# Performance work log

Measured on AMD Instinct MI355X. Metric: run time of the kernel, lower is better.

Reference implementation:

```python
import jax, jax.numpy as jnp
import numpy as np

N_NODES = 50000
N_EDGES = 600000
NODE_DIM = 128
HIDDEN = 128
LN_EPS = 1e-5


def setup_inputs() -> dict:
    key = jax.random.key(0)
    ks = jax.random.split(key, 12)
    x = jax.random.normal(ks[0], (N_NODES, NODE_DIM), dtype=jnp.float32)
    edge_index = jax.random.randint(ks[1], (2, N_EDGES), 0, N_NODES, dtype=jnp.int32)
    # GCNConv weights (glorot-ish scaling)
    W1 = jax.random.normal(ks[2], (NODE_DIM, HIDDEN), dtype=jnp.float32) / np.sqrt(NODE_DIM)
    b1 = jnp.zeros((HIDDEN,), jnp.float32)
    W2 = jax.random.normal(ks[3], (HIDDEN, HIDDEN), dtype=jnp.float32) / np.sqrt(HIDDEN)
    b2 = jnp.zeros((HIDDEN,), jnp.float32)
    g1 = jnp.ones((HIDDEN,), jnp.float32)
    beta1 = jnp.zeros((HIDDEN,), jnp.float32)
    g2 = jnp.ones((HIDDEN,), jnp.float32)
    beta2 = jnp.zeros((HIDDEN,), jnp.float32)
    return {"x": x, "edge_index": edge_index, "W1": W1, "b1": b1, "g1": g1,
            "beta1": beta1, "W2": W2, "b2": b2, "g2": g2, "beta2": beta2}


def _gcn_conv(x, src, dst, norm, W, b, n):
    # x' = sum_{j->i} norm_ji * (x_j @ W) + b   (self-loops already in src/dst)
    h = x @ W                                   # [N, H]
    msg = h[src] * norm[:, None]                # [E+N, H]
    out = jax.ops.segment_sum(msg, dst, num_segments=n)
    return out + b


def _layer_norm(x, gamma, beta):
    mu = jnp.mean(x, axis=-1, keepdims=True)
    var = jnp.mean((x - mu) ** 2, axis=-1, keepdims=True)
    return (x - mu) * jax.lax.rsqrt(var + LN_EPS) * gamma + beta


def reference(x, edge_index, W1, b1, g1, beta1, W2, b2, g2, beta2):
    n = x.shape[0]
    loop = jnp.arange(n, dtype=edge_index.dtype)
    src = jnp.concatenate([edge_index[0], loop])
    dst = jnp.concatenate([edge_index[1], loop])
    # symmetric normalization with self-loops (PyG GCNConv default)
    deg = jax.ops.segment_sum(jnp.ones_like(dst, dtype=x.dtype), dst, num_segments=n)
    dinv = jnp.where(deg > 0, jax.lax.rsqrt(jnp.maximum(deg, 1.0)), 0.0)
    norm = dinv[src] * dinv[dst]                # [E+N]

    h = _gcn_conv(x, src, dst, norm, W1, b1, n)
    h = _layer_norm(h, g1, beta1)
    h = jax.nn.relu(h)                          # relu between layers only
    h = _gcn_conv(h, src, dst, norm, W2, b2, n)
    h = _layer_norm(h, g2, beta2)
    return h
```

## Files before the change

kernel.cpp:

```cpp
#include <hip/hip_runtime.h>

#define DIM 128
#define LN_EPS 1e-5f

typedef __attribute__((ext_vector_type(8))) short bf16x8;
typedef __attribute__((ext_vector_type(4))) float f32x4;

static __device__ __forceinline__ unsigned short f2bf(float f) {
    unsigned int u = __builtin_bit_cast(unsigned int, f);
    u += 0x7fffu + ((u >> 16) & 1u);
    return (unsigned short)(u >> 16);
}
static __device__ __forceinline__ float bf2f_lo(unsigned int u) {
    return __builtin_bit_cast(float, u << 16);
}
static __device__ __forceinline__ float bf2f_hi(unsigned int u) {
    return __builtin_bit_cast(float, u & 0xffff0000u);
}

__global__ __launch_bounds__(256) void wt_count_kernel(const float* __restrict__ W1,
                                                       const float* __restrict__ W2,
                                                       unsigned short* __restrict__ Wt1,
                                                       unsigned short* __restrict__ Wt2,
                                                       const int* __restrict__ dst,
                                                       int* __restrict__ counts, int E) {
    int b = blockIdx.x;
    if (b < 128) {
        int elem = b * 256 + threadIdx.x;
        int which = elem >> 14;
        int rest = elem & 16383;
        int c = rest >> 7;
        int k = rest & 127;
        const float* W = which ? W2 : W1;
        unsigned short* Wt = which ? Wt2 : Wt1;
        Wt[c * 128 + k] = f2bf(W[k * 128 + c]);
    } else {
        int e = (b - 128) * 256 + threadIdx.x;
        if (e < E) atomicAdd(&counts[dst[e]], 1);
    }
}

__global__ __launch_bounds__(256) void scan1_kernel(const int* __restrict__ counts,
                                                    int* __restrict__ tmp,
                                                    int* __restrict__ bsums,
                                                    float* __restrict__ dinv, int n) {
    __shared__ int ts[256];
    int tid = threadIdx.x;
    int base = blockIdx.x * 1024 + tid * 4;
    int v[4];
#pragma unroll
    for (int j = 0; j < 4; ++j) {
        int i = base + j;
        v[j] = (i < n) ? counts[i] : 0;
        if (i < n) dinv[i] = rsqrtf((float)(v[j] + 1));
    }
    int s = v[0] + v[1] + v[2] + v[3];
    ts[tid] = s;
    __syncthreads();
    for (int off = 1; off < 256; off <<= 1) {
        int t2 = (tid >= off) ? ts[tid - off] : 0;
        __syncthreads();
        ts[tid] += t2;
        __syncthreads();
    }
    int excl = ts[tid] - s;
    int pre = excl;
#pragma unroll
    for (int j = 0; j < 4; ++j) {
        int i = base + j;
        if (i < n) tmp[i] = pre;
        pre += v[j];
    }
    if (tid == 255) bsums[blockIdx.x] = ts[255];
}

__global__ __launch_bounds__(256) void scan3_kernel(const int* __restrict__ tmp,
                                                    const int* __restrict__ bsums,
                                                    int* __restrict__ rowptr,
                                                    int* __restrict__ cursor,
                                                    int n, int E, int nb) {
    __shared__ int s_add;
    if (threadIdx.x < 64) {
        int lane = threadIdx.x;
        int v = (lane < nb) ? bsums[lane] : 0;
        int x = v;
#pragma unroll
        for (int off = 1; off < 64; off <<= 1) {
            int y = __shfl_up(x, off);
            if (lane >= off) x += y;
        }
        int excl = x - v;
        int mine = __builtin_amdgcn_readlane(excl, blockIdx.x);
        if (lane == 0) s_add = mine;
    }
    __syncthreads();
    int add = s_add;
    int base = blockIdx.x * 1024 + threadIdx.x * 4;
#pragma unroll
    for (int j = 0; j < 4; ++j) {
        int i = base + j;
        if (i < n) {
            int val = tmp[i] + add;
            rowptr[i] = val;
            cursor[i] = val;
        }
    }
    if (blockIdx.x == 0 && threadIdx.x == 0) rowptr[n] = E;
}

__global__ __launch_bounds__(256) void gemm1_fill_kernel(const float* __restrict__ A,
                                                         const unsigned short* __restrict__ Bt,
                                                         const float* __restrict__ dinv,
                                                         unsigned short* __restrict__ H,
                                                         int n, int ntiles, int gG,
                                                         const int* __restrict__ src,
                                                         const int* __restrict__ dst,
                                                         int* __restrict__ cursor,
                                                         unsigned short* __restrict__ colsrc,
                                                         int E) {
    __shared__ unsigned short Wlds[128 * 136];
    if (blockIdx.x >= gG) {
        int e = (blockIdx.x - gG) * 256 + threadIdx.x;
        if (e < E) {
            int p = atomicAdd(&cursor[dst[e]], 1);
            colsrc[p] = (unsigned short)src[e];
        }
        return;
    }
    for (int u = threadIdx.x; u < 2048; u += 256) {
        int row = u >> 4;
        int sub = u & 15;
        *(bf16x8*)&Wlds[row * 136 + sub * 8] = *(const bf16x8*)(Bt + row * 128 + sub * 8);
    }
    __syncthreads();

    int wid = threadIdx.x >> 6;
    int lane = threadIdx.x & 63;
    int tile = blockIdx.x * 4 + wid;
    if (tile >= ntiles) tile = ntiles - 1;
    int r0 = tile * 16;
    int mrow = lane & 15;
    int kgrp = lane >> 4;

    int arow_i = r0 + mrow;
    if (arow_i > n - 1) arow_i = n - 1;
    const float* arow = A + (size_t)arow_i * DIM + kgrp * 8;

    f32x4 acc[8];
#pragma unroll
    for (int t = 0; t < 8; ++t) acc[t] = (f32x4){0.f, 0.f, 0.f, 0.f};

#pragma unroll
    for (int kc = 0; kc < 4; ++kc) {
        float4 v0 = *(const float4*)(arow + kc * 32);
        float4 v1 = *(const float4*)(arow + kc * 32 + 4);
        bf16x8 af;
        af[0] = (short)f2bf(v0.x); af[1] = (short)f2bf(v0.y);
        af[2] = (short)f2bf(v0.z); af[3] = (short)f2bf(v0.w);
        af[4] = (short)f2bf(v1.x); af[5] = (short)f2bf(v1.y);
        af[6] = (short)f2bf(v1.z); af[7] = (short)f2bf(v1.w);
#pragma unroll
        for (int t = 0; t < 8; ++t) {
            bf16x8 bfv = *(const bf16x8*)&Wlds[(t * 16 + mrow) * 136 + kc * 32 + kgrp * 8];
            acc[t] = __builtin_amdgcn_mfma_f32_16x16x32_bf16(af, bfv, acc[t], 0, 0, 0);
        }
    }

    float dv[4];
#pragma unroll
    for (int reg = 0; reg < 4; ++reg) {
        int rr = r0 + kgrp * 4 + reg;
        dv[reg] = (rr < n) ? dinv[rr] : 0.f;
    }
#pragma unroll
    for (int t = 0; t < 8; ++t) {
#pragma unroll
        for (int reg = 0; reg < 4; ++reg) {
            int row = r0 + kgrp * 4 + reg;
            if (row < n) {
                int col = t * 16 + mrow;
                H[(size_t)row * DIM + col] = f2bf(acc[t][reg] * dv[reg]);
            }
        }
    }
}

__global__ __launch_bounds__(256) void gather_gemm_kernel(const int* __restrict__ rowptr,
                                                          const unsigned short* __restrict__ colsrc,
                                                          const uint4* __restrict__ H4,
                                                          const float* __restrict__ dinv,
                                                          const float* __restrict__ bias,
                                                          const float* __restrict__ gamma,
                                                          const float* __restrict__ beta,
                                                          const unsigned short* __restrict__ Wt2,
                                                          unsigned short* __restrict__ H2,
                                                          int n, int ntiles) {
    __shared__ unsigned short Wlds[128 * 136];
    __shared__ unsigned short Tl[4][16][136];
    for (int u = threadIdx.x; u < 2048; u += 256) {
        int row = u >> 4;
        int sub = u & 15;
        *(bf16x8*)&Wlds[row * 136 + sub * 8] = *(const bf16x8*)(Wt2 + row * 128 + sub * 8);
    }
    __syncthreads();

    int wid = threadIdx.x >> 6;
    int lane = threadIdx.x & 63;
    int tile = blockIdx.x * 4 + wid;
    if (tile >= ntiles) tile = ntiles - 1;
    int r0 = tile * 16;
    int grp = lane >> 4;
    int gl = lane & 15;

    float4 bb0 = ((const float4*)bias)[gl * 2];
    float4 bb1 = ((const float4*)bias)[gl * 2 + 1];
    float4 gg0 = ((const float4*)gamma)[gl * 2];
    float4 gg1 = ((const float4*)gamma)[gl * 2 + 1];
    float4 be0 = ((const float4*)beta)[gl * 2];
    float4 be1 = ((const float4*)beta)[gl * 2 + 1];

    for (int t = 0; t < 4; ++t) {
        int r = r0 + t * 4 + grp;
        int rc = (r < n) ? r : (n - 1);
        float di = dinv[rc];
        uint4 su = H4[(size_t)rc * 16 + gl];
        float a0 = bf2f_lo(su.x), a1 = bf2f_hi(su.x);
        float a2 = bf2f_lo(su.y), a3 = bf2f_hi(su.y);
        float a4 = bf2f_lo(su.z), a5 = bf2f_hi(su.z);
        float a6 = bf2f_lo(su.w), a7 = bf2f_hi(su.w);

        int p0 = rowptr[rc];
        int p1 = rowptr[rc + 1];
        int deg = p1 - p0;
        int m = max(deg, __shfl_xor(deg, 16));
        m = max(m, __shfl_xor(m, 32));
        int nch = (m + 15) >> 4;

        for (int c = 0; c < nch; ++c) {
            int cb = c * 16;
            int gi = p0 + cb + gl;
            gi = gi < p1 ? gi : p1 - 1;
            int idxv = (int)colsrc[gi];

            uint4 h[16];
#pragma unroll
            for (int j = 0; j < 16; ++j) {
                int s = __shfl(idxv, grp * 16 + j);
                h[j] = H4[(size_t)s * 16 + gl];
            }
#pragma unroll
            for (int j = 0; j < 16; ++j) {
                bool act = (cb + j < deg);
                a0 += act ? bf2f_lo(h[j].x) : 0.f;
                a1 += act ? bf2f_hi(h[j].x) : 0.f;
                a2 += act ? bf2f_lo(h[j].y) : 0.f;
                a3 += act ? bf2f_hi(h[j].y) : 0.f;
                a4 += act ? bf2f_lo(h[j].z) : 0.f;
                a5 += act ? bf2f_hi(h[j].z) : 0.f;
                a6 += act ? bf2f_lo(h[j].w) : 0.f;
                a7 += act ? bf2f_hi(h[j].w) : 0.f;
            }
        }

        float v0 = a0 * di + bb0.x;
        float v1 = a1 * di + bb0.y;
        float v2 = a2 * di + bb0.z;
        float v3 = a3 * di + bb0.w;
        float v4 = a4 * di + bb1.x;
        float v5 = a5 * di + bb1.y;
        float v6 = a6 * di + bb1.z;
        float v7 = a7 * di + bb1.w;

        float s1 = v0 + v1 + v2 + v3 + v4 + v5 + v6 + v7;
        float s2 = v0 * v0 + v1 * v1 + v2 * v2 + v3 * v3 +
                   v4 * v4 + v5 * v5 + v6 * v6 + v7 * v7;
#pragma unroll
        for (int off = 8; off > 0; off >>= 1) {
            s1 += __shfl_xor(s1, off);
            s2 += __shfl_xor(s2, off);
        }
        float mu = s1 * (1.f / 128.f);
        float var = s2 * (1.f / 128.f) - mu * mu;
        float rstd = rsqrtf(var + LN_EPS);

        float o0 = fmaxf((v0 - mu) * rstd * gg0.x + be0.x, 0.f);
        float o1 = fmaxf((v1 - mu) * rstd * gg0.y + be0.y, 0.f);
        float o2 = fmaxf((v2 - mu) * rstd * gg0.z + be0.z, 0.f);
        float o3 = fmaxf((v3 - mu) * rstd * gg0.w + be0.w, 0.f);
        float o4 = fmaxf((v4 - mu) * rstd * gg1.x + be1.x, 0.f);
        float o5 = fmaxf((v5 - mu) * rstd * gg1.y + be1.y, 0.f);
        float o6 = fmaxf((v6 - mu) * rstd * gg1.z + be1.z, 0.f);
        float o7 = fmaxf((v7 - mu) * rstd * gg1.w + be1.w, 0.f);

        bf16x8 pk;
        pk[0] = (short)f2bf(o0); pk[1] = (short)f2bf(o1);
        pk[2] = (short)f2bf(o2); pk[3] = (short)f2bf(o3);
        pk[4] = (short)f2bf(o4); pk[5] = (short)f2bf(o5);
        pk[6] = (short)f2bf(o6); pk[7] = (short)f2bf(o7);
        *(bf16x8*)&Tl[wid][t * 4 + grp][gl * 8] = pk;
    }

    __syncthreads();

    int mrow = lane & 15;
    int kg = lane >> 4;
    f32x4 acc[8];
#pragma unroll
    for (int t = 0; t < 8; ++t) acc[t] = (f32x4){0.f, 0.f, 0.f, 0.f};

#pragma unroll
    for (int kc = 0; kc < 4; ++kc) {
        bf16x8 af = *(const bf16x8*)&Tl[wid][mrow][kc * 32 + kg * 8];
#pragma unroll
        for (int t = 0; t < 8; ++t) {
            bf16x8 bfv = *(const bf16x8*)&Wlds[(t * 16 + mrow) * 136 + kc * 32 + kg * 8];
            acc[t] = __builtin_amdgcn_mfma_f32_16x16x32_bf16(af, bfv, acc[t], 0, 0, 0);
        }
    }

    float dv[4];
#pragma unroll
    for (int reg = 0; reg < 4; ++reg) {
        int rr = r0 + kg * 4 + reg;
        dv[reg] = (rr < n) ? dinv[rr] : 0.f;
    }
#pragma unroll
    for (int t = 0; t < 8; ++t) {
#pragma unroll
        for (int reg = 0; reg < 4; ++reg) {
            int row = r0 + kg * 4 + reg;
            if (row < n) {
                int col = t * 16 + mrow;
                H2[(size_t)row * DIM + col] = f2bf(acc[t][reg] * dv[reg]);
            }
        }
    }
}

__global__ __launch_bounds__(256) void gather_ln_kernel(const int* __restrict__ rowptr,
                                                        const unsigned short* __restrict__ colsrc,
                                                        const uint2* __restrict__ H2,
                                                        const float* __restrict__ dinv,
                                                        const float* __restrict__ bias,
                                                        const float* __restrict__ gamma,
                                                        const float* __restrict__ beta,
                                                        uint2* __restrict__ out_bf,
                                                        float* __restrict__ out_f,
                                                        int n, int relu) {
    int wid = threadIdx.x >> 6;
    int lane = threadIdx.x & 63;
    int half = lane >> 5;
    int hl = lane & 31;
    int r = blockIdx.x * 8 + wid * 2 + half;
    int valid = (r < n);
    int rc = valid ? r : (n - 1);

    float di = dinv[rc];
    float4 bb = ((const float4*)bias)[hl];
    float4 gg = ((const float4*)gamma)[hl];
    float4 be = ((const float4*)beta)[hl];

    uint2 su = H2[(size_t)rc * 32 + hl];
    float a0 = bf2f_lo(su.x), a1 = bf2f_hi(su.x);
    float a2 = bf2f_lo(su.y), a3 = bf2f_hi(su.y);

    int p0 = rowptr[rc];
    int p1 = rowptr[rc + 1];
    int deg = p1 - p0;
    int maxd = max(deg, __shfl_xor(deg, 32));
    int nchunks = (maxd + 15) >> 4;
    int hbase = half << 5;

    for (int c = 0; c < nchunks; ++c) {
        int cbase = c * 16;
        int gi = p0 + cbase + hl;
        gi = gi < p1 ? gi : p1 - 1;
        int idxv = (int)colsrc[gi];

        uint2 h[16];
#pragma unroll
        for (int j = 0; j < 16; ++j) {
            int s = __shfl(idxv, hbase + j);
            h[j] = H2[(size_t)s * 32 + hl];
        }
#pragma unroll
        for (int j = 0; j < 16; ++j) {
            bool act = (cbase + j < deg);
            a0 += act ? bf2f_lo(h[j].x) : 0.f;
            a1 += act ? bf2f_hi(h[j].x) : 0.f;
            a2 += act ? bf2f_lo(h[j].y) : 0.f;
            a3 += act ? bf2f_hi(h[j].y) : 0.f;
        }
    }

    float v0 = a0 * di + bb.x;
    float v1 = a1 * di + bb.y;
    float v2 = a2 * di + bb.z;
    float v3 = a3 * di + bb.w;

    float s1 = v0 + v1 + v2 + v3;
    float s2 = v0 * v0 + v1 * v1 + v2 * v2 + v3 * v3;
#pragma unroll
    for (int off = 16; off > 0; off >>= 1) {
        s1 += __shfl_xor(s1, off);
        s2 += __shfl_xor(s2, off);
    }
    float mu = s1 * (1.f / 128.f);
    float var = s2 * (1.f / 128.f) - mu * mu;
    float rstd = rsqrtf(var + LN_EPS);

    float o0 = (v0 - mu) * rstd * gg.x + be.x;
    float o1 = (v1 - mu) * rstd * gg.y + be.y;
    float o2 = (v2 - mu) * rstd * gg.z + be.z;
    float o3 = (v3 - mu) * rstd * gg.w + be.w;
    if (relu) {
        o0 = fmaxf(o0, 0.f); o1 = fmaxf(o1, 0.f);
        o2 = fmaxf(o2, 0.f); o3 = fmaxf(o3, 0.f);
    }
    if (valid) {
        if (out_bf) {
            uint2 pk;
            pk.x = (unsigned int)f2bf(o0) | ((unsigned int)f2bf(o1) << 16);
            pk.y = (unsigned int)f2bf(o2) | ((unsigned int)f2bf(o3) << 16);
            out_bf[(size_t)r * 32 + hl] = pk;
        } else {
            ((float4*)out_f)[(size_t)r * 32 + hl] = make_float4(o0, o1, o2, o3);
        }
    }
}

extern "C" void kernel_launch(void* const* d_in, const int* in_sizes, int n_in,
                              void* d_out, int out_size, void* d_ws, size_t ws_size,
                              hipStream_t stream) {
    const float* x   = (const float*)d_in[0];
    const int*   ei  = (const int*)d_in[1];
    const float* W1  = (const float*)d_in[2];
    const float* b1  = (const float*)d_in[3];
    const float* g1  = (const float*)d_in[4];
    const float* be1 = (const float*)d_in[5];
    const float* W2  = (const float*)d_in[6];
    const float* b2  = (const float*)d_in[7];
    const float* g2  = (const float*)d_in[8];
    const float* be2 = (const float*)d_in[9];

    int n = in_sizes[0] / DIM;
    int E = in_sizes[1] / 2;
    const int* src = ei;
    const int* dst = ei + E;

    char* wp = (char*)d_ws;
    auto alloc = [&](size_t bytes) {
        void* p = (void*)wp;
        wp += (bytes + 255) & ~(size_t)255;
        return p;
    };
    float*          dinv   = (float*)alloc((size_t)n * 4);
    int*            counts = (int*)alloc((size_t)n * 4);
    int*            tmp    = (int*)alloc((size_t)n * 4);
    int*            rowptr = (int*)alloc((size_t)(n + 1) * 4);
    int*            cursor = (int*)alloc((size_t)n * 4);
    int*            bsums  = (int*)alloc(64 * 4);
    unsigned short* colsrc = (unsigned short*)alloc((size_t)E * 2);
    unsigned short* Wt1    = (unsigned short*)alloc(128 * 128 * 2);
    unsigned short* Wt2    = (unsigned short*)alloc(128 * 128 * 2);
    unsigned short* H      = (unsigned short*)alloc((size_t)n * DIM * 2);
    unsigned short* H2     = (unsigned short*)alloc((size_t)n * DIM * 2);

    hipMemsetAsync(counts, 0, (size_t)n * 4, stream);

    int gE = (E + 255) / 256;
    wt_count_kernel<<<128 + gE, 256, 0, stream>>>(W1, W2, Wt1, Wt2, dst, counts, E);

    int nb1 = (n + 1023) / 1024;
    scan1_kernel<<<nb1, 256, 0, stream>>>(counts, tmp, bsums, dinv, n);
    scan3_kernel<<<nb1, 256, 0, stream>>>(tmp, bsums, rowptr, cursor, n, E, nb1);

    int ntiles = (n + 15) / 16;
    int gG = (ntiles + 3) / 4;

    gemm1_fill_kernel<<<gG + gE, 256, 0, stream>>>(x, Wt1, dinv, H, n, ntiles, gG,
                                                   src, dst, cursor, colsrc, E);

    gather_gemm_kernel<<<gG, 256, 0, stream>>>(rowptr, colsrc, (const uint4*)H, dinv,
                                               b1, g1, be1, Wt2, H2, n, ntiles);

    int gA = (n + 7) / 8;
    gather_ln_kernel<<<gA, 256, 0, stream>>>(rowptr, colsrc, (const uint2*)H2, dinv,
                                             b2, g2, be2, nullptr, (float*)d_out, n, 0);
}
```

Measured before the change: 233.4 us.

## Fuse scan kernels with grid sync, shrink gather_gemm blocks, widen final gather

The two prefix-scan kernels become one, where the last block to finish computes the block offsets and the other blocks spin on a flag, so one launch and the tmp round-trip go away. gather_gemm drops the full 34KB W2 copy in LDS and uses 128-thread blocks over 16 rows, with each wave reading half of W2 straight from global memory; this targets higher occupancy at the cost of redundant global reads. The final gather reads 16-byte loads (8 bf16 per lane) with 16 lanes per row instead of 8-byte loads. Bias, gamma and beta loads are moved to where they are used to lower register pressure. The spin-wait relies on all scan blocks being resident at once, which holds for the roughly 49 blocks used here.

```diff
diff --git a/kernel.cpp b/kernel.cpp
--- a/kernel.cpp
+++ b/kernel.cpp
@@ -40,13 +40,18 @@
     }
 }
 
-__global__ __launch_bounds__(256) void scan1_kernel(const int* __restrict__ counts,
-                                                    int* __restrict__ tmp,
-                                                    int* __restrict__ bsums,
-                                                    float* __restrict__ dinv, int n) {
+__global__ __launch_bounds__(256) void scan_fused_kernel(const int* __restrict__ counts,
+                                                         int* __restrict__ bsums,
+                                                         int* __restrict__ bpref,
+                                                         int* __restrict__ sync2,
+                                                         int* __restrict__ rowptr,
+                                                         int* __restrict__ cursor,
+                                                         float* __restrict__ dinv,
+                                                         int n, int E, int nb) {
     __shared__ int ts[256];
     int tid = threadIdx.x;
-    int base = blockIdx.x * 1024 + tid * 4;
+    int b = blockIdx.x;
+    int base = b * 1024 + tid * 4;
     int v[4];
 #pragma unroll
     for (int j = 0; j < 4; ++j) {
@@ -64,48 +69,40 @@
         __syncthreads();
     }
     int excl = ts[tid] - s;
-    int pre = excl;
-#pragma unroll
-    for (int j = 0; j < 4; ++j) {
-        int i = base + j;
-        if (i < n) tmp[i] = pre;
-        pre += v[j];
-    }
-    if (tid == 255) bsums[blockIdx.x] = ts[255];
-}
-
-__global__ __launch_bounds__(256) void scan3_kernel(const int* __restrict__ tmp,
-                                                    const int* __restrict__ bsums,
-                                                    int* __restrict__ rowptr,
-                                                    int* __restrict__ cursor,
-                                                    int n, int E, int nb) {
-    __shared__ int s_add;
-    if (threadIdx.x < 64) {
-        int lane = threadIdx.x;
-        int v = (lane < nb) ? bsums[lane] : 0;
-        int x = v;
-#pragma unroll
-        for (int off = 1; off < 64; off <<= 1) {
-            int y = __shfl_up(x, off);
-            if (lane >= off) x += y;
-        }
-        int excl = x - v;
-        int mine = __builtin_amdgcn_readlane(excl, blockIdx.x);
-        if (lane == 0) s_add = mine;
+
+    if (tid == 255) {
+        bsums[b] = ts[255];
+        __threadfence();
+        int t = atomicAdd(&sync2[0], 1);
+        if (t == nb - 1) {
+            __threadfence();
+            int acc = 0;
+            for (int k = 0; k < nb; ++k) {
+                int sv = bsums[k];
+                bpref[k] = acc;
+                acc += sv;
+            }
+            __threadfence();
+            atomicExch(&sync2[1], 1);
+        }
+    }
+    if (tid == 0) {
+        while (atomicAdd(&sync2[1], 0) == 0) { __builtin_amdgcn_s_sleep(8); }
     }
     __syncthreads();
-    int add = s_add;
-    int base = blockIdx.x * 1024 + threadIdx.x * 4;
+    __threadfence();
+
+    int pre = bpref[b] + excl;
 #pragma unroll
     for (int j = 0; j < 4; ++j) {
         int i = base + j;
         if (i < n) {
-            int val = tmp[i] + add;
-            rowptr[i] = val;
-            cursor[i] = val;
-        }
-    }
-    if (blockIdx.x == 0 && threadIdx.x == 0) rowptr[n] = E;
+            rowptr[i] = pre;
+            cursor[i] = pre;
+        }
+        pre += v[j];
+    }
+    if (b == 0 && tid == 0) rowptr[n] = E;
 }
 
 __global__ __launch_bounds__(256) void gemm1_fill_kernel(const float* __restrict__ A,
@@ -185,52 +182,36 @@
     }
 }
 
-__global__ __launch_bounds__(256) void gather_gemm_kernel(const int* __restrict__ rowptr,
-                                                          const unsigned short* __restrict__ colsrc,
-                                                          const uint4* __restrict__ H4,
-                                                          const float* __restrict__ dinv,
-                                                          const float* __restrict__ bias,
-                                                          const float* __restrict__ gamma,
-                                                          const float* __restrict__ beta,
-                                                          const unsigned short* __restrict__ Wt2,
-                                                          unsigned short* __restrict__ H2,
-                                                          int n, int ntiles) {
-    __shared__ unsigned short Wlds[128 * 136];
-    __shared__ unsigned short Tl[4][16][136];
-    for (int u = threadIdx.x; u < 2048; u += 256) {
-        int row = u >> 4;
-        int sub = u & 15;
-        *(bf16x8*)&Wlds[row * 136 + sub * 8] = *(const bf16x8*)(Wt2 + row * 128 + sub * 8);
-    }
-    __syncthreads();
-
+__global__ __launch_bounds__(128, 5) void gather_gemm_kernel(const int* __restrict__ rowptr,
+                                                             const unsigned short* __restrict__ colsrc,
+                                                             const uint4* __restrict__ H4,
+                                                             const float* __restrict__ dinv,
+                                                             const float* __restrict__ bias,
+                                                             const float* __restrict__ gamma,
+                                                             const float* __restrict__ beta,
+                                                             const unsigned short* __restrict__ Wt2,
+                                                             unsigned short* __restrict__ H2,
+                                                             int n) {
+    __shared__ unsigned short Tl[16][136];
     int wid = threadIdx.x >> 6;
     int lane = threadIdx.x & 63;
-    int tile = blockIdx.x * 4 + wid;
-    if (tile >= ntiles) tile = ntiles - 1;
-    int r0 = tile * 16;
+    int r0 = blockIdx.x * 16;
     int grp = lane >> 4;
     int gl = lane & 15;
 
-    float4 bb0 = ((const float4*)bias)[gl * 2];
-    float4 bb1 = ((const float4*)bias)[gl * 2 + 1];
-    float4 gg0 = ((const float4*)gamma)[gl * 2];
-    float4 gg1 = ((const float4*)gamma)[gl * 2 + 1];
-    float4 be0 = ((const float4*)beta)[gl * 2];
-    float4 be1 = ((const float4*)beta)[gl * 2 + 1];
-
-    for (int t = 0; t < 4; ++t) {
-        int r = r0 + t * 4 + grp;
+#pragma unroll
+    for (int t = 0; t < 2; ++t) {
+        int r = r0 + wid * 8 + t * 4 + grp;
         int rc = (r < n) ? r : (n - 1);
         float di = dinv[rc];
         uint4 su = H4[(size_t)rc * 16 + gl];
+        int p0 = rowptr[rc];
+        int p1 = rowptr[rc + 1];
         float a0 = bf2f_lo(su.x), a1 = bf2f_hi(su.x);
         float a2 = bf2f_lo(su.y), a3 = bf2f_hi(su.y);
         float a4 = bf2f_lo(su.z), a5 = bf2f_hi(su.z);
         float a6 = bf2f_lo(su.w), a7 = bf2f_hi(su.w);
 
-        int p0 = rowptr[rc];
-        int p1 = rowptr[rc + 1];
         int deg = p1 - p0;
         int m = max(deg, __shfl_xor(deg, 16));
         m = max(m, __shfl_xor(m, 32));
@@ -245,8 +226,8 @@
             uint4 h[16];
 #pragma unroll
             for (int j = 0; j < 16; ++j) {
-                int s = __shfl(idxv, grp * 16 + j);
-                h[j] = H4[(size_t)s * 16 + gl];
+                int sS = __shfl(idxv, grp * 16 + j);
+                h[j] = H4[(size_t)sS * 16 + gl];
             }
 #pragma unroll
             for (int j = 0; j < 16; ++j) {
@@ -262,6 +243,8 @@
             }
         }
 
+        float4 bb0 = ((const float4*)bias)[gl * 2];
+        float4 bb1 = ((const float4*)bias)[gl * 2 + 1];
         float v0 = a0 * di + bb0.x;
         float v1 = a1 * di + bb0.y;
         float v2 = a2 * di + bb0.z;
@@ -283,6 +266,11 @@
         float var = s2 * (1.f / 128.f) - mu * mu;
         float rstd = rsqrtf(var + LN_EPS);
 
+        float4 gg0 = ((const float4*)gamma)[gl * 2];
+        float4 gg1 = ((const float4*)gamma)[gl * 2 + 1];
+        float4 be0 = ((const float4*)beta)[gl * 2];
+        float4 be1 = ((const float4*)beta)[gl * 2 + 1];
+
         float o0 = fmaxf((v0 - mu) * rstd * gg0.x + be0.x, 0.f);
         float o1 = fmaxf((v1 - mu) * rstd * gg0.y + be0.y, 0.f);
         float o2 = fmaxf((v2 - mu) * rstd * gg0.z + be0.z, 0.f);
@@ -297,24 +285,25 @@
         pk[2] = (short)f2bf(o2); pk[3] = (short)f2bf(o3);
         pk[4] = (short)f2bf(o4); pk[5] = (short)f2bf(o5);
         pk[6] = (short)f2bf(o6); pk[7] = (short)f2bf(o7);
-        *(bf16x8*)&Tl[wid][t * 4 + grp][gl * 8] = pk;
+        *(bf16x8*)&Tl[wid * 8 + t * 4 + grp][gl * 8] = pk;
     }
 
     __syncthreads();
 
     int mrow = lane & 15;
     int kg = lane >> 4;
-    f32x4 acc[8];
-#pragma unroll
-    for (int t = 0; t < 8; ++t) acc[t] = (f32x4){0.f, 0.f, 0.f, 0.f};
+    f32x4 acc[4];
+#pragma unroll
+    for (int tt = 0; tt < 4; ++tt) acc[tt] = (f32x4){0.f, 0.f, 0.f, 0.f};
 
 #pragma unroll
     for (int kc = 0; kc < 4; ++kc) {
-        bf16x8 af = *(const bf16x8*)&Tl[wid][mrow][kc * 32 + kg * 8];
-#pragma unroll
-        for (int t = 0; t < 8; ++t) {
-            bf16x8 bfv = *(const bf16x8*)&Wlds[(t * 16 + mrow) * 136 + kc * 32 + kg * 8];
-            acc[t] = __builtin_amdgcn_mfma_f32_16x16x32_bf16(af, bfv, acc[t], 0, 0, 0);
+        bf16x8 af = *(const bf16x8*)&Tl[mrow][kc * 32 + kg * 8];
+#pragma unroll
+        for (int tt = 0; tt < 4; ++tt) {
+            int trow = (wid * 4 + tt) * 16 + mrow;
+            bf16x8 bv = *(const bf16x8*)(Wt2 + (size_t)trow * 128 + kc * 32 + kg * 8);
+            acc[tt] = __builtin_amdgcn_mfma_f32_16x16x32_bf16(af, bv, acc[tt], 0, 0, 0);
         }
     }
 
@@ -325,83 +314,91 @@
         dv[reg] = (rr < n) ? dinv[rr] : 0.f;
     }
 #pragma unroll
-    for (int t = 0; t < 8; ++t) {
+    for (int tt = 0; tt < 4; ++tt) {
 #pragma unroll
         for (int reg = 0; reg < 4; ++reg) {
             int row = r0 + kg * 4 + reg;
             if (row < n) {
-                int col = t * 16 + mrow;
-                H2[(size_t)row * DIM + col] = f2bf(acc[t][reg] * dv[reg]);
+                int col = (wid * 4 + tt) * 16 + mrow;
+                H2[(size_t)row * DIM + col] = f2bf(acc[tt][reg] * dv[reg]);
             }
         }
     }
 }
 
-__global__ __launch_bounds__(256) void gather_ln_kernel(const int* __restrict__ rowptr,
-                                                        const unsigned short* __restrict__ colsrc,
-                                                        const uint2* __restrict__ H2,
-                                                        const float* __restrict__ dinv,
-                                                        const float* __restrict__ bias,
-                                                        const float* __restrict__ gamma,
-                                                        const float* __restrict__ beta,
-                                                        uint2* __restrict__ out_bf,
-                                                        float* __restrict__ out_f,
-                                                        int n, int relu) {
+__global__ __launch_bounds__(256, 5) void gather_out_kernel(const int* __restrict__ rowptr,
+                                                            const unsigned short* __restrict__ colsrc,
+                                                            const uint4* __restrict__ H4,
+                                                            const float* __restrict__ dinv,
+                                                            const float* __restrict__ bias,
+                                                            const float* __restrict__ gamma,
+                                                            const float* __restrict__ beta,
+                                                            float* __restrict__ out,
+                                                            int n) {
     int wid = threadIdx.x >> 6;
     int lane = threadIdx.x & 63;
-    int half = lane >> 5;
-    int hl = lane & 31;
-    int r = blockIdx.x * 8 + wid * 2 + half;
+    int grp = lane >> 4;
+    int gl = lane & 15;
+    int r = blockIdx.x * 16 + wid * 4 + grp;
     int valid = (r < n);
     int rc = valid ? r : (n - 1);
 
     float di = dinv[rc];
-    float4 bb = ((const float4*)bias)[hl];
-    float4 gg = ((const float4*)gamma)[hl];
-    float4 be = ((const float4*)beta)[hl];
-
-    uint2 su = H2[(size_t)rc * 32 + hl];
+    uint4 su = H4[(size_t)rc * 16 + gl];
+    int p0 = rowptr[rc];
+    int p1 = rowptr[rc + 1];
     float a0 = bf2f_lo(su.x), a1 = bf2f_hi(su.x);
     float a2 = bf2f_lo(su.y), a3 = bf2f_hi(su.y);
-
-    int p0 = rowptr[rc];
-    int p1 = rowptr[rc + 1];
+    float a4 = bf2f_lo(su.z), a5 = bf2f_hi(su.z);
+    float a6 = bf2f_lo(su.w), a7 = bf2f_hi(su.w);
+
     int deg = p1 - p0;
-    int maxd = max(deg, __shfl_xor(deg, 32));
-    int nchunks = (maxd + 15) >> 4;
-    int hbase = half << 5;
-
-    for (int c = 0; c < nchunks; ++c) {
-        int cbase = c * 16;
-        int gi = p0 + cbase + hl;
+    int m = max(deg, __shfl_xor(deg, 16));
+    m = max(m, __shfl_xor(m, 32));
+    int nch = (m + 15) >> 4;
+
+    for (int c = 0; c < nch; ++c) {
+        int cb = c * 16;
+        int gi = p0 + cb + gl;
         gi = gi < p1 ? gi : p1 - 1;
         int idxv = (int)colsrc[gi];
 
-        uint2 h[16];
+        uint4 h[16];
 #pragma unroll
         for (int j = 0; j < 16; ++j) {
-            int s = __shfl(idxv, hbase + j);
-            h[j] = H2[(size_t)s * 32 + hl];
+            int sS = __shfl(idxv, grp * 16 + j);
+            h[j] = H4[(size_t)sS * 16 + gl];
         }
 #pragma unroll
         for (int j = 0; j < 16; ++j) {
-            bool act = (cbase + j < deg);
+            bool act = (cb + j < deg);
             a0 += act ? bf2f_lo(h[j].x) : 0.f;
             a1 += act ? bf2f_hi(h[j].x) : 0.f;
             a2 += act ? bf2f_lo(h[j].y) : 0.f;
             a3 += act ? bf2f_hi(h[j].y) : 0.f;
-        }
-    }
-
-    float v0 = a0 * di + bb.x;
-    float v1 = a1 * di + bb.y;
-    float v2 = a2 * di + bb.z;
-    float v3 = a3 * di + bb.w;
-
-    float s1 = v0 + v1 + v2 + v3;
-    float s2 = v0 * v0 + v1 * v1 + v2 * v2 + v3 * v3;
-#pragma unroll
-    for (int off = 16; off > 0; off >>= 1) {
+            a4 += act ? bf2f_lo(h[j].z) : 0.f;
+            a5 += act ? bf2f_hi(h[j].z) : 0.f;
+            a6 += act ? bf2f_lo(h[j].w) : 0.f;
+            a7 += act ? bf2f_hi(h[j].w) : 0.f;
+        }
+    }
+
+    float4 bb0 = ((const float4*)bias)[gl * 2];
+    float4 bb1 = ((const float4*)bias)[gl * 2 + 1];
+    float v0 = a0 * di + bb0.x;
+    float v1 = a1 * di + bb0.y;
+    float v2 = a2 * di + bb0.z;
+    float v3 = a3 * di + bb0.w;
+    float v4 = a4 * di + bb1.x;
+    float v5 = a5 * di + bb1.y;
+    float v6 = a6 * di + bb1.z;
+    float v7 = a7 * di + bb1.w;
+
+    float s1 = v0 + v1 + v2 + v3 + v4 + v5 + v6 + v7;
+    float s2 = v0 * v0 + v1 * v1 + v2 * v2 + v3 * v3 +
+               v4 * v4 + v5 * v5 + v6 * v6 + v7 * v7;
+#pragma unroll
+    for (int off = 8; off > 0; off >>= 1) {
         s1 += __shfl_xor(s1, off);
         s2 += __shfl_xor(s2, off);
     }
@@ -409,23 +406,23 @@
     float var = s2 * (1.f / 128.f) - mu * mu;
     float rstd = rsqrtf(var + LN_EPS);
 
-    float o0 = (v0 - mu) * rstd * gg.x + be.x;
-    float o1 = (v1 - mu) * rstd * gg.y + be.y;
-    float o2 = (v2 - mu) * rstd * gg.z + be.z;
-    float o3 = (v3 - mu) * rstd * gg.w + be.w;
-    if (relu) {
-        o0 = fmaxf(o0, 0.f); o1 = fmaxf(o1, 0.f);
-        o2 = fmaxf(o2, 0.f); o3 = fmaxf(o3, 0.f);
-    }
+    float4 gg0 = ((const float4*)gamma)[gl * 2];
+    float4 gg1 = ((const float4*)gamma)[gl * 2 + 1];
+    float4 be0 = ((const float4*)beta)[gl * 2];
+    float4 be1 = ((const float4*)beta)[gl * 2 + 1];
+
+    float o0 = (v0 - mu) * rstd * gg0.x + be0.x;
+    float o1 = (v1 - mu) * rstd * gg0.y + be0.y;
+    float o2 = (v2 - mu) * rstd * gg0.z + be0.z;
+    float o3 = (v3 - mu) * rstd * gg0.w + be0.w;
+    float o4 = (v4 - mu) * rstd * gg1.x + be1.x;
+    float o5 = (v5 - mu) * rstd * gg1.y + be1.y;
+    float o6 = (v6 - mu) * rstd * gg1.z + be1.z;
+    float o7 = (v7 - mu) * rstd * gg1.w + be1.w;
+
     if (valid) {
-        if (out_bf) {
-            uint2 pk;
-            pk.x = (unsigned int)f2bf(o0) | ((unsigned int)f2bf(o1) << 16);
-            pk.y = (unsigned int)f2bf(o2) | ((unsigned int)f2bf(o3) << 16);
-            out_bf[(size_t)r * 32 + hl] = pk;
-        } else {
-            ((float4*)out_f)[(size_t)r * 32 + hl] = make_float4(o0, o1, o2, o3);
-        }
+        ((float4*)out)[(size_t)r * 32 + gl * 2] = make_float4(o0, o1, o2, o3);
+        ((float4*)out)[(size_t)r * 32 + gl * 2 + 1] = make_float4(o4, o5, o6, o7);
     }
 }
 
@@ -455,25 +452,26 @@
         return p;
     };
     float*          dinv   = (float*)alloc((size_t)n * 4);
-    int*            counts = (int*)alloc((size_t)n * 4);
-    int*            tmp    = (int*)alloc((size_t)n * 4);
+    int*            counts = (int*)alloc((size_t)(n + 64) * 4);
+    int*            sync2  = counts + n;
     int*            rowptr = (int*)alloc((size_t)(n + 1) * 4);
     int*            cursor = (int*)alloc((size_t)n * 4);
-    int*            bsums  = (int*)alloc(64 * 4);
+    int*            bsums  = (int*)alloc(256 * 4);
+    int*            bpref  = (int*)alloc(256 * 4);
     unsigned short* colsrc = (unsigned short*)alloc((size_t)E * 2);
     unsigned short* Wt1    = (unsigned short*)alloc(128 * 128 * 2);
     unsigned short* Wt2    = (unsigned short*)alloc(128 * 128 * 2);
     unsigned short* H      = (unsigned short*)alloc((size_t)n * DIM * 2);
     unsigned short* H2     = (unsigned short*)alloc((size_t)n * DIM * 2);
 
-    hipMemsetAsync(counts, 0, (size_t)n * 4, stream);
+    hipMemsetAsync(counts, 0, (size_t)(n + 64) * 4, stream);
 
     int gE = (E + 255) / 256;
     wt_count_kernel<<<128 + gE, 256, 0, stream>>>(W1, W2, Wt1, Wt2, dst, counts, E);
 
     int nb1 = (n + 1023) / 1024;
-    scan1_kernel<<<nb1, 256, 0, stream>>>(counts, tmp, bsums, dinv, n);
-    scan3_kernel<<<nb1, 256, 0, stream>>>(tmp, bsums, rowptr, cursor, n, E, nb1);
+    scan_fused_kernel<<<nb1, 256, 0, stream>>>(counts, bsums, bpref, sync2,
+                                               rowptr, cursor, dinv, n, E, nb1);
 
     int ntiles = (n + 15) / 16;
     int gG = (ntiles + 3) / 4;
@@ -481,10 +479,9 @@
     gemm1_fill_kernel<<<gG + gE, 256, 0, stream>>>(x, Wt1, dinv, H, n, ntiles, gG,
                                                    src, dst, cursor, colsrc, E);
 
-    gather_gemm_kernel<<<gG, 256, 0, stream>>>(rowptr, colsrc, (const uint4*)H, dinv,
-                                               b1, g1, be1, Wt2, H2, n, ntiles);
-
-    int gA = (n + 7) / 8;
-    gather_ln_kernel<<<gA, 256, 0, stream>>>(rowptr, colsrc, (const uint2*)H2, dinv,
-                                             b2, g2, be2, nullptr, (float*)d_out, n, 0);
-}
+    gather_gemm_kernel<<<ntiles, 128, 0, stream>>>(rowptr, colsrc, (const uint4*)H, dinv,
+                                                   b1, g1, be1, Wt2, H2, n);
+
+    gather_out_kernel<<<ntiles, 256, 0, stream>>>(rowptr, colsrc, (const uint4*)H2, dinv,
+                                                  b2, g2, be2, (float*)d_out, n);
+}
```

Result: slower. 246.4 us (+5.6%).
